# Kernel optimization log

Measured on AMD Instinct MI355X. Metric: run time of the kernel, lower is better.

The kernel has to match this reference:

```python
import jax, jax.numpy as jnp
import numpy as np

MID = 256

def setup_inputs() -> dict:
    key = jax.random.key(0)
    ks = jax.random.split(key, 6)
    s = 1.0 / np.sqrt(MID)
    u = lambda k, shape: jax.random.uniform(k, shape, jnp.float32, -s, s)
    return {
        "W_ih": u(ks[0], (4 * MID, 2)),
        "W_hh": u(ks[1], (4 * MID, MID)),
        "b_ih": u(ks[2], (4 * MID,)),
        "b_hh": u(ks[3], (4 * MID,)),
        "W_out": u(ks[4], (1, MID)),
        "b_out": u(ks[5], (1,)),
        "sequence_dim": 48,
        "sequence_num": 512,
    }

def reference(W_ih, W_hh, b_ih, b_hh, W_out, b_out, sequence_dim, sequence_num):
    # obs is 2-D -> torch nn.LSTM treats it as UNBATCHED: (L=sequence_num, H_in=2),
    # hidden state (mid,) per layer, carried across outer iterations.
    N = sequence_num
    mid = W_hh.shape[1]
    b = b_ih + b_hh  # fuse the two LSTM biases

    def lstm(hc, obs):
        # obs: (N, 2) time-major unbatched sequence
        def step(carry, x):
            h, c = carry
            g = W_ih @ x + W_hh @ h + b          # (4*mid,)
            i, f, gg, o = jnp.split(g, 4)         # torch gate order i,f,g,o
            c = jax.nn.sigmoid(f) * c + jax.nn.sigmoid(i) * jnp.tanh(gg)
            h = jax.nn.sigmoid(o) * jnp.tanh(c)
            return (h, c), h
        hc, hs = jax.lax.scan(step, hc, obs)
        return hc, hs                              # hs: (N, mid)

    def outer(carry, k):
        hc, samp, prob = carry
        obs = jnp.concatenate([samp, prob], axis=1)  # (N, 2)
        hc, hs = lstm(hc, obs)
        p = jax.nn.sigmoid(hs @ W_out.T + b_out)     # (N, 1)
        smp = jax.random.bernoulli(k, p).astype(p.dtype)
        lp = smp * jnp.log(p) + (1.0 - smp) * jnp.log1p(-p)        # Bernoulli log_prob
        ent = -(p * jnp.log(p) + (1.0 - p) * jnp.log1p(-p))        # Bernoulli entropy
        return (hc, smp, p), (smp[:, 0], lp[:, 0], ent[:, 0])

    key = jax.random.key(42)
    keys = jax.random.split(key, sequence_dim - 1)
    h0 = (jnp.zeros((mid,), W_hh.dtype), jnp.zeros((mid,), W_hh.dtype))
    z = jnp.zeros((N, 1), W_hh.dtype)
    _, (ss, lps, ents) = jax.lax.scan(outer, (h0, z, z), keys)

    samples = jnp.concatenate([jnp.zeros((1, N), ss.dtype), ss], axis=0)  # (T, N)
    samples = samples.T.astype(jnp.int32)                                  # (N, T)
    logprobs = lps.sum(0)
    logprobs = logprobs - logprobs.mean()
    entropies = ents.mean(0)
    return samples, logprobs, entropies
```

## Files before the change

### kernel.cpp

```cpp
#include <hip/hip_runtime.h>
#include <stdint.h>


#define MID      256
#define NOUT     48
#define NSEQ     512
#define NOUTER   47
#define NSTEP    (NOUTER * NSEQ)
#define NBLK     16
#define MAGIC_V  0x1234ABCDu
#define LOG2E    1.4426950408889634f

typedef __attribute__((ext_vector_type(4))) float f32x4;

#define LD_REL(p) __hip_atomic_load((p), __ATOMIC_RELAXED, __HIP_MEMORY_SCOPE_AGENT)

#define LDS_BARRIER() do {                                          \
    asm volatile("s_waitcnt lgkmcnt(0)\n\ts_barrier" ::: "memory"); \
    __builtin_amdgcn_sched_barrier(0);                              \
  } while (0)

__device__ __forceinline__ uint32_t rotl32(uint32_t x, int d) {
  return (x << d) | (x >> (32 - d));
}

__device__ __forceinline__ void threefry2x32(uint32_t k0, uint32_t k1,
                                             uint32_t x0, uint32_t x1,
                                             uint32_t& o0, uint32_t& o1) {
  uint32_t ks2 = k0 ^ k1 ^ 0x1BD11BDAu;
  uint32_t v0 = x0 + k0, v1 = x1 + k1;
#define TF_R(r) { v0 += v1; v1 = rotl32(v1, r); v1 ^= v0; }
  TF_R(13) TF_R(15) TF_R(26) TF_R(6)
  v0 += k1;  v1 += ks2 + 1u;
  TF_R(17) TF_R(29) TF_R(16) TF_R(24)
  v0 += ks2; v1 += k0 + 2u;
  TF_R(13) TF_R(15) TF_R(26) TF_R(6)
  v0 += k0;  v1 += k1 + 3u;
  TF_R(17) TF_R(29) TF_R(16) TF_R(24)
  v0 += k1;  v1 += ks2 + 4u;
  TF_R(13) TF_R(15) TF_R(26) TF_R(6)
  v0 += ks2; v1 += k0 + 5u;
#undef TF_R
  o0 = v0; o1 = v1;
}

__device__ __forceinline__ float sigf(float x) { return 1.0f / (1.0f + expf(-x)); }

__device__ __forceinline__ uint64_t packht(float h, uint32_t tag) {
  return ((uint64_t)tag << 32) | (uint64_t)__float_as_uint(h);
}

__global__ __launch_bounds__(256, 1)
void arlstm_kernel(const float* __restrict__ W_ih, const float* __restrict__ W_hh,
                   const float* __restrict__ b_ih, const float* __restrict__ b_hh,
                   const float* __restrict__ W_out, const float* __restrict__ b_out,
                   float* __restrict__ out, uint64_t* __restrict__ ws) {
  uint64_t* h_hist = ws;
  float*    obsbuf = (float*)(ws + 512 * 256);
  uint32_t* p_prog = (uint32_t*)(obsbuf + 2 * 512 * 2);
  uint32_t* magic  = p_prog + 16;
  uint64_t* ob64   = (uint64_t*)obsbuf;

  const int tid = threadIdx.x;
  const int blk = blockIdx.x;

  __shared__ __align__(16) float hstage[256];
  __shared__ float plds[4][64];
  __shared__ float ring[2][16][2];
  __shared__ float lp_acc[512];
  __shared__ float ent_acc[512];
  __shared__ float red[256];

  if (blk == NBLK) {
    __hip_atomic_store(&h_hist[tid], 0ull, __ATOMIC_RELAXED, __HIP_MEMORY_SCOPE_AGENT);
    if (tid < 16)
      __hip_atomic_store(&p_prog[tid], 0u, __ATOMIC_RELAXED, __HIP_MEMORY_SCOPE_AGENT);
    out[(tid)       * NOUT] = 0.0f;
    out[(tid + 256) * NOUT] = 0.0f;
    lp_acc[tid] = 0.0f;  lp_acc[tid + 256] = 0.0f;
    ent_acc[tid] = 0.0f; ent_acc[tid + 256] = 0.0f;
    __threadfence();
    __syncthreads();
    if (tid == 0)
      __hip_atomic_store(magic, MAGIC_V, __ATOMIC_RELEASE, __HIP_MEMORY_SCOPE_AGENT);

    const int w    = tid >> 6;
    const int lane = tid & 63;
    const float wo0 = W_out[lane * 4 + 0], wo1 = W_out[lane * 4 + 1];
    const float wo2 = W_out[lane * 4 + 2], wo3 = W_out[lane * 4 + 3];
    const float bo = b_out[0];

    for (int s = w + 1; s <= NSTEP; s += 4) {
      const int k = (s - 1) >> 9;
      const int t = (s - 1) & 511;
      uint64_t* src = h_hist + (uint64_t)(s & 511) * 256 + lane * 4;
      uint64_t v0, v1, v2, v3;
      for (;;) {
        v0 = LD_REL(src + 0);
        v1 = LD_REL(src + 1);
        v2 = LD_REL(src + 2);
        v3 = LD_REL(src + 3);
        int ok = ((uint32_t)(v0 >> 32) == (uint32_t)s) &
                 ((uint32_t)(v1 >> 32) == (uint32_t)s) &
                 ((uint32_t)(v2 >> 32) == (uint32_t)s) &
                 ((uint32_t)(v3 >> 32) == (uint32_t)s);
        if (__all(ok)) break;
      }
      float zp = fmaf(__uint_as_float((uint32_t)v0), wo0,
                 fmaf(__uint_as_float((uint32_t)v1), wo1,
                 fmaf(__uint_as_float((uint32_t)v2), wo2,
                      __uint_as_float((uint32_t)v3) * wo3)));
      zp += __shfl_xor(zp, 1);
      zp += __shfl_xor(zp, 2);
      zp += __shfl_xor(zp, 4);
      zp += __shfl_xor(zp, 8);
      zp += __shfl_xor(zp, 16);
      zp += __shfl_xor(zp, 32);
      const float p = sigf(zp + bo);

      uint32_t ka, kb, c1, c2;
      threefry2x32(0u, 42u, 0u, (uint32_t)k, ka, kb);
      threefry2x32(ka, kb, 0u, (uint32_t)t, c1, c2);
      const uint32_t bits = c1 ^ c2;
      const float u = __uint_as_float((bits >> 9) | 0x3f800000u) - 1.0f;
      const float smp = (u < p) ? 1.0f : 0.0f;

      if (lane == 0) {
        uint32_t* ob = (uint32_t*)(obsbuf + ((k + 1) & 1) * (512 * 2) + t * 2);
        __hip_atomic_store(&ob[0], __float_as_uint(smp), __ATOMIC_RELAXED, __HIP_MEMORY_SCOPE_AGENT);
        __hip_atomic_store(&ob[1], __float_as_uint(p),   __ATOMIC_RELAXED, __HIP_MEMORY_SCOPE_AGENT);
        __hip_atomic_store(&p_prog[w], (uint32_t)s, __ATOMIC_RELEASE, __HIP_MEMORY_SCOPE_AGENT);
        out[t * NOUT + (k + 1)] = smp;
        const float lg = logf(p), lg1 = log1pf(-p);
        lp_acc[t]  += (smp > 0.5f) ? lg : lg1;
        ent_acc[t] -= (p * lg + (1.0f - p) * lg1);
      }
    }
    __syncthreads();
    red[tid] = lp_acc[tid] + lp_acc[tid + 256];
    __syncthreads();
    for (int off = 128; off > 0; off >>= 1) {
      if (tid < off) red[tid] += red[tid + off];
      __syncthreads();
    }
    const float mean = red[0] * (1.0f / 512.0f);
    out[24576 + tid]        = lp_acc[tid]        - mean;
    out[24576 + 256 + tid]  = lp_acc[tid + 256]  - mean;
    out[25088 + tid]        = ent_acc[tid]       * (1.0f / 47.0f);
    out[25088 + 256 + tid]  = ent_acc[tid + 256] * (1.0f / 47.0f);
  } else {
    const int part = tid >> 6;
    const int r    = tid & 63;
    const int gate = r >> 4;
    const int jloc = r & 15;
    const int row  = gate * 256 + blk * 16 + jloc;

    f32x4 w4[16];
    const f32x4* wsrc = (const f32x4*)(W_hh + row * 256 + part * 64);
#pragma unroll
    for (int i = 0; i < 16; ++i) w4[i] = wsrc[i];
#pragma unroll
    for (int i = 0; i < 16; ++i) asm volatile("" : "+v"(w4[i]));

    float bb = 0.f, wx0 = 0.f, wx1 = 0.f, mconst = 0.f, ml = 0.f, ad = 0.f;
    if (tid < 64) {
      const int g4 = tid >> 4;
      const int rr = g4 * 256 + blk * 16 + (tid & 15);
      bb  = b_ih[rr] + b_hh[rr];
      wx0 = W_ih[rr * 2 + 0];
      wx1 = W_ih[rr * 2 + 1];
      mconst = (g4 == 2) ? (-2.0f * LOG2E) : (-LOG2E);
      ml     = (g4 == 2) ? 2.0f : 1.0f;
      ad     = (g4 == 2) ? -1.0f : 0.0f;
    }

    if (tid < 16) {
      ring[0][tid][0] = 0.f; ring[0][tid][1] = 0.f;
      ring[1][tid][0] = 0.f; ring[1][tid][1] = 0.f;
    }

    if (tid == 0) {
      while (__hip_atomic_load(magic, __ATOMIC_ACQUIRE, __HIP_MEMORY_SCOPE_AGENT) != MAGIC_V) {}
    }
    __syncthreads();

    float c_st = 0.0f;
    const int jglob = blk * 16 + (tid & 15);
    const bool own = (tid >= blk * 16) && (tid < blk * 16 + 16);

    int      pf_tgt = 0, pf_need = 0;
    uint32_t pf_ppv = 0;
    uint64_t pf_ov  = 0;

    for (int s = 1; s <= NSTEP; ++s) {
      const int ph = (s - 1) & 15;

      if (part == 3) {
        if (ph == 0) {
          pf_tgt  = s + 16 + r;
          pf_need = 0;
          if (r < 16 && pf_tgt > NSEQ && pf_tgt <= NSTEP) {
            pf_need = pf_tgt - NSEQ;
            pf_ppv  = LD_REL(&p_prog[(pf_need - 1) & 3]);
          }
        } else if (ph == 1) {
          bool ok = (pf_need == 0) || (pf_ppv >= (uint32_t)pf_need);
          while (!__all(ok)) {
            if (!ok) pf_ppv = LD_REL(&p_prog[(pf_need - 1) & 3]);
            ok = (pf_need == 0) || (pf_ppv >= (uint32_t)pf_need);
          }
          pf_ov = 0;
          if (r < 16 && pf_need != 0) {
            const int kk = (pf_tgt - 1) >> 9;
            const int tt = (pf_tgt - 1) & 511;
            pf_ov = LD_REL(ob64 + (kk & 1) * 512 + tt);
          }
        } else if (ph == 2) {
          if (r < 16) {
            const int par = (((s - 3) >> 4) + 1) & 1;
            ring[par][r][0] = __uint_as_float((uint32_t)pf_ov);
            ring[par][r][1] = __uint_as_float((uint32_t)(pf_ov >> 32));
          }
        }
      }

      if (s == 1 || !own) {
        uint64_t* src = h_hist + (uint64_t)((s - 1) & 511) * 256 + tid;
        const uint32_t want = (uint32_t)(s - 1);
        uint64_t v = LD_REL(src);
        if ((uint32_t)(v >> 32) != want) {
          uint64_t q0 = LD_REL(src), q1 = LD_REL(src);
          uint64_t q2 = LD_REL(src), q3 = LD_REL(src);
          for (;;) {
            if ((uint32_t)(q0 >> 32) == want) { v = q0; break; }
            q0 = LD_REL(src);
            if ((uint32_t)(q1 >> 32) == want) { v = q1; break; }
            q1 = LD_REL(src);
            if ((uint32_t)(q2 >> 32) == want) { v = q2; break; }
            q2 = LD_REL(src);
            if ((uint32_t)(q3 >> 32) == want) { v = q3; break; }
            q3 = LD_REL(src);
          }
        }
        hstage[tid] = __uint_as_float((uint32_t)v);
      }
      LDS_BARRIER();

      float a0 = 0.f, a1 = 0.f, a2 = 0.f, a3 = 0.f;
      const f32x4* hs4 = (const f32x4*)(hstage + part * 64);
#pragma unroll
      for (int i = 0; i < 16; ++i) {
        const f32x4 hv = hs4[i];
        a0 = fmaf(w4[i][0], hv[0], a0);
        a1 = fmaf(w4[i][1], hv[1], a1);
        a2 = fmaf(w4[i][2], hv[2], a2);
        a3 = fmaf(w4[i][3], hv[3], a3);
      }
      plds[part][r] = (a0 + a1) + (a2 + a3);
      LDS_BARRIER();

      if (tid < 64) {
        const float sx = ring[((s - 1) >> 4) & 1][ph][0];
        const float px = ring[((s - 1) >> 4) & 1][ph][1];
        const float base = wx0 * sx + wx1 * px + bb;
        const float gv = ((plds[0][tid] + plds[1][tid]) +
                          (plds[2][tid] + plds[3][tid])) + base;
        const float e   = __builtin_amdgcn_exp2f(gv * mconst);
        const float y   = __builtin_amdgcn_rcpf(1.0f + e);
        const float act = __builtin_fmaf(ml, y, ad);
        const int j = tid & 15;
        const float a_f = __shfl(act, j + 16, 64);
        const float a_g = __shfl(act, j + 32, 64);
        const float a_o = __shfl(act, j + 48, 64);
        if (tid < 16) {
          const float t1 = a_f * c_st;
          const float t2 = act * a_g;
          c_st = t1 + t2;
          const float ec = __builtin_amdgcn_exp2f(c_st * (-2.0f * LOG2E));
          const float yc = __builtin_amdgcn_rcpf(1.0f + ec);
          const float th = __builtin_fmaf(2.0f, yc, -1.0f);
          const float hnew = a_o * th;
          hstage[jglob] = hnew;
          __hip_atomic_store(&h_hist[(uint64_t)(s & 511) * 256 + jglob],
                             packht(hnew, (uint32_t)s),
                             __ATOMIC_RELAXED, __HIP_MEMORY_SCOPE_AGENT);
        }
      }
    }
  }
}

extern "C" void kernel_launch(void* const* d_in, const int* in_sizes, int n_in,
                              void* d_out, int out_size, void* d_ws, size_t ws_size,
                              hipStream_t stream) {
  const float* W_ih  = (const float*)d_in[0];
  const float* W_hh  = (const float*)d_in[1];
  const float* b_ih  = (const float*)d_in[2];
  const float* b_hh  = (const float*)d_in[3];
  const float* W_out = (const float*)d_in[4];
  const float* b_out = (const float*)d_in[5];
  float* out = (float*)d_out;
  uint64_t* ws = (uint64_t*)d_ws;

  arlstm_kernel<<<dim3(NBLK + 1), dim3(256), 0, stream>>>(
      W_ih, W_hh, b_ih, b_hh, W_out, b_out, out, ws);
}
```

Before: 32.57 ms.

## Make each wavefront an independent LSTM unit group, removing block barriers

Each of the four wavefronts in a block now owns four hidden units across all four gates. The K-dimension partial sums are reduced with cross-lane shuffles instead of through LDS, so the two per-step workgroup barriers become plain LDS waitcnt fences. Each wave polls the global hidden-state history itself, four values per lane, into its own double-buffered, padded LDS copy, and runs its own prefetch of observations. The aim is to cut intra-block synchronization from the serial critical path. The cost is four times the global polling traffic, since every wave reads the whole state.

```diff
diff --git a/kernel.cpp b/kernel.cpp
--- a/kernel.cpp
+++ b/kernel.cpp
@@ -10,14 +10,15 @@
 #define NBLK     16
 #define MAGIC_V  0x1234ABCDu
 #define LOG2E    1.4426950408889634f
+#define QSTRIDE  72
 
 typedef __attribute__((ext_vector_type(4))) float f32x4;
 
 #define LD_REL(p) __hip_atomic_load((p), __ATOMIC_RELAXED, __HIP_MEMORY_SCOPE_AGENT)
 
-#define LDS_BARRIER() do {                                          \
-    asm volatile("s_waitcnt lgkmcnt(0)\n\ts_barrier" ::: "memory"); \
-    __builtin_amdgcn_sched_barrier(0);                              \
+#define LGKM_FENCE() do {                                   \
+    asm volatile("s_waitcnt lgkmcnt(0)" ::: "memory");      \
+    __builtin_amdgcn_sched_barrier(0);                      \
   } while (0)
 
 __device__ __forceinline__ uint32_t rotl32(uint32_t x, int d) {
@@ -64,9 +65,8 @@
   const int tid = threadIdx.x;
   const int blk = blockIdx.x;
 
-  __shared__ __align__(16) float hstage[256];
-  __shared__ float plds[4][64];
-  __shared__ float ring[2][16][2];
+  __shared__ __align__(16) float hst[4][2][4 * QSTRIDE];
+  __shared__ float ring[4][2][16][2];
   __shared__ float lp_acc[512];
   __shared__ float ent_acc[512];
   __shared__ float red[256];
@@ -149,34 +149,37 @@
     out[25088 + tid]        = ent_acc[tid]       * (1.0f / 47.0f);
     out[25088 + 256 + tid]  = ent_acc[tid + 256] * (1.0f / 47.0f);
   } else {
-    const int part = tid >> 6;
-    const int r    = tid & 63;
-    const int gate = r >> 4;
-    const int jloc = r & 15;
-    const int row  = gate * 256 + blk * 16 + jloc;
+    const int w    = tid >> 6;
+    const int lane = tid & 63;
+    const int q    = lane & 3;
+    const int jj   = (lane >> 2) & 3;
+    const int g    = lane >> 4;
+    const int jglob = blk * 16 + 4 * w + jj;
+    const int row   = g * 256 + blk * 16 + 4 * w + jj;
+    const int Lown  = 4 * blk + w;
 
     f32x4 w4[16];
-    const f32x4* wsrc = (const f32x4*)(W_hh + row * 256 + part * 64);
+    const f32x4* wsrc = (const f32x4*)(W_hh + row * 256 + q * 64);
 #pragma unroll
     for (int i = 0; i < 16; ++i) w4[i] = wsrc[i];
 #pragma unroll
     for (int i = 0; i < 16; ++i) asm volatile("" : "+v"(w4[i]));
 
-    float bb = 0.f, wx0 = 0.f, wx1 = 0.f, mconst = 0.f, ml = 0.f, ad = 0.f;
-    if (tid < 64) {
-      const int g4 = tid >> 4;
-      const int rr = g4 * 256 + blk * 16 + (tid & 15);
-      bb  = b_ih[rr] + b_hh[rr];
-      wx0 = W_ih[rr * 2 + 0];
-      wx1 = W_ih[rr * 2 + 1];
-      mconst = (g4 == 2) ? (-2.0f * LOG2E) : (-LOG2E);
-      ml     = (g4 == 2) ? 2.0f : 1.0f;
-      ad     = (g4 == 2) ? -1.0f : 0.0f;
-    }
-
-    if (tid < 16) {
-      ring[0][tid][0] = 0.f; ring[0][tid][1] = 0.f;
-      ring[1][tid][0] = 0.f; ring[1][tid][1] = 0.f;
+    const float bb  = b_ih[row] + b_hh[row];
+    const float wx0 = W_ih[row * 2 + 0];
+    const float wx1 = W_ih[row * 2 + 1];
+    const float mconst = (g == 2) ? (-2.0f * LOG2E) : (-LOG2E);
+    const float ml     = (g == 2) ? 2.0f : 1.0f;
+    const float ad     = (g == 2) ? -1.0f : 0.0f;
+
+    {
+      f32x4 z = {0.f, 0.f, 0.f, 0.f};
+      *(f32x4*)&hst[w][1][(lane >> 4) * QSTRIDE + (lane & 15) * 4] = z;
+      *(f32x4*)&hst[w][0][(lane >> 4) * QSTRIDE + (lane & 15) * 4] = z;
+      if (lane < 16) {
+        ring[w][0][lane][0] = 0.f; ring[w][0][lane][1] = 0.f;
+        ring[w][1][lane][0] = 0.f; ring[w][1][lane][1] = 0.f;
+      }
     }
 
     if (tid == 0) {
@@ -185,8 +188,6 @@
     __syncthreads();
 
     float c_st = 0.0f;
-    const int jglob = blk * 16 + (tid & 15);
-    const bool own = (tid >= blk * 16) && (tid < blk * 16 + 16);
 
     int      pf_tgt = 0, pf_need = 0;
     uint32_t pf_ppv = 0;
@@ -195,59 +196,62 @@
     for (int s = 1; s <= NSTEP; ++s) {
       const int ph = (s - 1) & 15;
 
-      if (part == 3) {
-        if (ph == 0) {
-          pf_tgt  = s + 16 + r;
-          pf_need = 0;
-          if (r < 16 && pf_tgt > NSEQ && pf_tgt <= NSTEP) {
-            pf_need = pf_tgt - NSEQ;
-            pf_ppv  = LD_REL(&p_prog[(pf_need - 1) & 3]);
-          }
-        } else if (ph == 1) {
-          bool ok = (pf_need == 0) || (pf_ppv >= (uint32_t)pf_need);
-          while (!__all(ok)) {
-            if (!ok) pf_ppv = LD_REL(&p_prog[(pf_need - 1) & 3]);
-            ok = (pf_need == 0) || (pf_ppv >= (uint32_t)pf_need);
-          }
-          pf_ov = 0;
-          if (r < 16 && pf_need != 0) {
-            const int kk = (pf_tgt - 1) >> 9;
-            const int tt = (pf_tgt - 1) & 511;
-            pf_ov = LD_REL(ob64 + (kk & 1) * 512 + tt);
-          }
-        } else if (ph == 2) {
-          if (r < 16) {
-            const int par = (((s - 3) >> 4) + 1) & 1;
-            ring[par][r][0] = __uint_as_float((uint32_t)pf_ov);
-            ring[par][r][1] = __uint_as_float((uint32_t)(pf_ov >> 32));
-          }
-        }
-      }
-
-      if (s == 1 || !own) {
-        uint64_t* src = h_hist + (uint64_t)((s - 1) & 511) * 256 + tid;
+      if (ph == 0) {
+        pf_tgt  = s + 16 + lane;
+        pf_need = 0;
+        if (lane < 16 && pf_tgt > NSEQ && pf_tgt <= NSTEP) {
+          pf_need = pf_tgt - NSEQ;
+          pf_ppv  = LD_REL(&p_prog[(pf_need - 1) & 3]);
+        }
+      } else if (ph == 1) {
+        bool ok = (pf_need == 0) || (pf_ppv >= (uint32_t)pf_need);
+        while (!__all(ok)) {
+          if (!ok) pf_ppv = LD_REL(&p_prog[(pf_need - 1) & 3]);
+          ok = (pf_need == 0) || (pf_ppv >= (uint32_t)pf_need);
+        }
+        pf_ov = 0;
+        if (lane < 16 && pf_need != 0) {
+          const int kk = (pf_tgt - 1) >> 9;
+          const int tt = (pf_tgt - 1) & 511;
+          pf_ov = LD_REL(ob64 + (kk & 1) * 512 + tt);
+        }
+      } else if (ph == 2) {
+        if (lane < 16) {
+          const int par = (((s - 3) >> 4) + 1) & 1;
+          ring[w][par][lane][0] = __uint_as_float((uint32_t)pf_ov);
+          ring[w][par][lane][1] = __uint_as_float((uint32_t)(pf_ov >> 32));
+        }
+      }
+
+      if (s > 1) {
+        uint64_t* src = h_hist + (uint64_t)((s - 1) & 511) * 256 + 4 * lane;
         const uint32_t want = (uint32_t)(s - 1);
-        uint64_t v = LD_REL(src);
-        if ((uint32_t)(v >> 32) != want) {
-          uint64_t q0 = LD_REL(src), q1 = LD_REL(src);
-          uint64_t q2 = LD_REL(src), q3 = LD_REL(src);
-          for (;;) {
-            if ((uint32_t)(q0 >> 32) == want) { v = q0; break; }
-            q0 = LD_REL(src);
-            if ((uint32_t)(q1 >> 32) == want) { v = q1; break; }
-            q1 = LD_REL(src);
-            if ((uint32_t)(q2 >> 32) == want) { v = q2; break; }
-            q2 = LD_REL(src);
-            if ((uint32_t)(q3 >> 32) == want) { v = q3; break; }
-            q3 = LD_REL(src);
-          }
-        }
-        hstage[tid] = __uint_as_float((uint32_t)v);
-      }
-      LDS_BARRIER();
+        uint64_t v0, v1, v2, v3;
+        for (;;) {
+          v0 = LD_REL(src + 0);
+          v1 = LD_REL(src + 1);
+          v2 = LD_REL(src + 2);
+          v3 = LD_REL(src + 3);
+          int ok = (lane == Lown) |
+                   (((uint32_t)(v0 >> 32) == want) &
+                    ((uint32_t)(v1 >> 32) == want) &
+                    ((uint32_t)(v2 >> 32) == want) &
+                    ((uint32_t)(v3 >> 32) == want));
+          if (__all(ok)) break;
+        }
+        if (lane != Lown) {
+          f32x4 hw;
+          hw[0] = __uint_as_float((uint32_t)v0);
+          hw[1] = __uint_as_float((uint32_t)v1);
+          hw[2] = __uint_as_float((uint32_t)v2);
+          hw[3] = __uint_as_float((uint32_t)v3);
+          *(f32x4*)&hst[w][s & 1][(lane >> 4) * QSTRIDE + (lane & 15) * 4] = hw;
+        }
+      }
+      LGKM_FENCE();
 
       float a0 = 0.f, a1 = 0.f, a2 = 0.f, a3 = 0.f;
-      const f32x4* hs4 = (const f32x4*)(hstage + part * 64);
+      const f32x4* hs4 = (const f32x4*)&hst[w][s & 1][q * QSTRIDE];
 #pragma unroll
       for (int i = 0; i < 16; ++i) {
         const f32x4 hv = hs4[i];
@@ -256,31 +260,33 @@
         a2 = fmaf(w4[i][2], hv[2], a2);
         a3 = fmaf(w4[i][3], hv[3], a3);
       }
-      plds[part][r] = (a0 + a1) + (a2 + a3);
-      LDS_BARRIER();
-
-      if (tid < 64) {
-        const float sx = ring[((s - 1) >> 4) & 1][ph][0];
-        const float px = ring[((s - 1) >> 4) & 1][ph][1];
-        const float base = wx0 * sx + wx1 * px + bb;
-        const float gv = ((plds[0][tid] + plds[1][tid]) +
-                          (plds[2][tid] + plds[3][tid])) + base;
-        const float e   = __builtin_amdgcn_exp2f(gv * mconst);
-        const float y   = __builtin_amdgcn_rcpf(1.0f + e);
-        const float act = __builtin_fmaf(ml, y, ad);
-        const int j = tid & 15;
-        const float a_f = __shfl(act, j + 16, 64);
-        const float a_g = __shfl(act, j + 32, 64);
-        const float a_o = __shfl(act, j + 48, 64);
-        if (tid < 16) {
-          const float t1 = a_f * c_st;
-          const float t2 = act * a_g;
-          c_st = t1 + t2;
-          const float ec = __builtin_amdgcn_exp2f(c_st * (-2.0f * LOG2E));
-          const float yc = __builtin_amdgcn_rcpf(1.0f + ec);
-          const float th = __builtin_fmaf(2.0f, yc, -1.0f);
-          const float hnew = a_o * th;
-          hstage[jglob] = hnew;
+      float gp = (a0 + a1) + (a2 + a3);
+      gp += __shfl_xor(gp, 1);
+      gp += __shfl_xor(gp, 2);
+
+      const float sx = ring[w][((s - 1) >> 4) & 1][ph][0];
+      const float px = ring[w][((s - 1) >> 4) & 1][ph][1];
+      const float base = wx0 * sx + wx1 * px + bb;
+      const float gv = gp + base;
+
+      const float e   = __builtin_amdgcn_exp2f(gv * mconst);
+      const float y   = __builtin_amdgcn_rcpf(1.0f + e);
+      const float act = __builtin_fmaf(ml, y, ad);
+
+      const float a_f = __shfl(act, (lane & 15) + 16, 64);
+      const float a_g = __shfl(act, (lane & 15) + 32, 64);
+      const float a_o = __shfl(act, (lane & 15) + 48, 64);
+
+      if (g == 0) {
+        const float t1 = a_f * c_st;
+        const float t2 = act * a_g;
+        c_st = t1 + t2;
+        const float ec = __builtin_amdgcn_exp2f(c_st * (-2.0f * LOG2E));
+        const float yc = __builtin_amdgcn_rcpf(1.0f + ec);
+        const float th = __builtin_fmaf(2.0f, yc, -1.0f);
+        const float hnew = a_o * th;
+        if (q == 0) {
+          hst[w][(s + 1) & 1][(jglob >> 6) * QSTRIDE + (jglob & 63)] = hnew;
           __hip_atomic_store(&h_hist[(uint64_t)(s & 511) * 256 + jglob],
                              packht(hnew, (uint32_t)s),
                              __ATOMIC_RELAXED, __HIP_MEMORY_SCOPE_AGENT);
```

Result: slower. 43.72 ms (+34.3%).
